# Kernel tuning notes

Hardware: AMD Instinct MI355X
Metric: run time of the kernel (lower is better)

Reference implementation:

```python
import jax, jax.numpy as jnp
import numpy as np
from jax import lax

B, L_IN, D, D_INNER = 4, 1024, 512, 512
H, DK = 8, 64
WIN = [4, 4, 4]
INNER_SIZE = 5   # temporal intra-level neighborhood size
SEM_K = 32       # opt.semantic_node: topk per level for semantic mask
N_LAYER = 2


def _build_temporal_mask(input_size, window_size, inner_size):
    # faithful port of Encoder.get_mask (Pyraformer-Naive mask)
    all_size = [input_size]
    for w in window_size:
        all_size.append(all_size[-1] // w)
    L = sum(all_size)
    m = np.zeros((L, L), dtype=np.float32)
    iw = inner_size // 2
    starts = [sum(all_size[:i]) for i in range(len(all_size))]
    for li, n in enumerate(all_size):
        st = starts[li]
        for i in range(st, st + n):
            m[i, max(i - iw, st):min(i + iw + 1, st + n)] = 1
    for li in range(1, len(all_size)):
        st = starts[li]
        prev = all_size[li - 1]
        w = window_size[li - 1]
        for i in range(st, st + all_size[li]):
            ls = st - prev + (i - st) * w
            rs = st if i == st + all_size[li] - 1 else st - prev + (i - st + 1) * w
            m[i, ls:rs] = 1
            m[ls:rs, i] = 1
    return (1 - m).astype(bool), all_size

TMASK_NP, ALL_SIZE = _build_temporal_mask(L_IN, WIN, INNER_SIZE)
L_TOT = sum(ALL_SIZE)  # 1360


def _ln(x, g, b, eps):
    mu = jnp.mean(x, axis=-1, keepdims=True)
    var = jnp.mean(jnp.square(x - mu), axis=-1, keepdims=True)
    return (x - mu) * lax.rsqrt(var + eps) * g + b


def _mha(x, Wq, Wk, Wv, fcW, fcb, g, b, mask):
    # post-norm MHA (normalize_before=False), dropout disabled (eval)
    Bq, L, _ = x.shape
    q = (x @ Wq).reshape(Bq, L, H, DK)
    k = (x @ Wk).reshape(Bq, L, H, DK)
    v = (x @ Wv).reshape(Bq, L, H, DK)
    a = jnp.einsum('bqhd,bkhd->bhqk', q, k) / np.float32(DK ** 0.5)
    a = jnp.where(mask, -jnp.inf, a)
    p = jax.nn.softmax(a, axis=-1)
    o = jnp.einsum('bhqk,bkhd->bqhd', p, v).reshape(Bq, L, H * DK)
    return _ln(o @ fcW + fcb + x, g, b, 1e-6)


def _semantic_mask(x):
    # get_semantic_mask: per-level cosine similarity, mask topk-most-similar within each level
    nrm = jnp.linalg.norm(x, axis=-1, keepdims=True)
    xn = x / jnp.maximum(nrm, 1e-8)
    sim = jnp.einsum('bid,bjd->bij', xn, xn)
    Bq = x.shape[0]
    mask = jnp.zeros((Bq, L_TOT, L_TOT), dtype=bool)
    bidx = jnp.arange(Bq)[:, None, None]
    start = 0
    for n in ALL_SIZE:
        k = min(n, SEM_K)
        blk = sim[:, start:start + n, start:start + n]
        idx = lax.top_k(blk, k)[1]              # [B, n, k]
        ridx = jnp.arange(n)[None, :, None]
        bm = jnp.zeros((Bq, n, n), dtype=bool).at[bidx, ridx, idx].set(True)
        mask = mask.at[:, start:start + n, start:start + n].set(bm)
        start += n
    return mask


def _bottleneck(x, dW, db, cW, cb, uW, ub, g, b):
    t = jnp.transpose(x @ dW + db, (0, 2, 1))  # [B, d_inner, L]
    outs = []
    for i in range(len(WIN)):
        t = lax.conv_general_dilated(t, cW[i], (WIN[i],), 'VALID',
                                     dimension_numbers=('NCH', 'OIH', 'NCH')) + cb[i][None, :, None]
        t = t / np.float32(np.sqrt(1.0 + 1e-5))  # eval BatchNorm with identity running stats
        t = jax.nn.elu(t)
        outs.append(t)
    pyr = jnp.transpose(jnp.concatenate(outs, axis=2), (0, 2, 1)) @ uW + ub
    return _ln(jnp.concatenate([x, pyr], axis=1), g, b, 1e-5)


def _forward(x_enc, down_W, down_b, conv_W, conv_b, up_W, up_b, bc_ln_g, bc_ln_b,
             attn_Wq, attn_Wk, attn_Wv, attn_fcW, attn_fcb, attn_ln_g, attn_ln_b,
             ffn_W1, ffn_b1, ffn_W2, ffn_b2, ffn_ln_g, ffn_ln_b):
    tmask = jnp.asarray(TMASK_NP)[None, None]  # [1,1,Lt,Lt]
    x = _bottleneck(x_enc, down_W, down_b, conv_W, conv_b, up_W, up_b, bc_ln_g, bc_ln_b)
    for l in range(N_LAYER):
        res = x
        t_out = _mha(x, attn_Wq[l, 0], attn_Wk[l, 0], attn_Wv[l, 0], attn_fcW[l, 0],
                     attn_fcb[l, 0], attn_ln_g[l, 0], attn_ln_b[l, 0], tmask)
        smask = _semantic_mask(x)[:, None]     # [B,1,Lt,Lt]
        s_out = _mha(x, attn_Wq[l, 1], attn_Wk[l, 1], attn_Wv[l, 1], attn_fcW[l, 1],
                     attn_fcb[l, 1], attn_ln_g[l, 1], attn_ln_b[l, 1], smask)
        x = (t_out + s_out + res) / 3.0
        res = x
        h = jax.nn.relu(x @ ffn_W1[l] + ffn_b1[l])
        x = _ln(h @ ffn_W2[l] + ffn_b2[l] + res, ffn_ln_g[l], ffn_ln_b[l], 1e-6)
    return x


def setup_inputs() -> dict:
    key = jax.random.key(0)
    ks = jax.random.split(key, 16)
    s = 0.02
    inp = {
        'x_enc': jax.random.normal(ks[0], (B, L_IN, D), jnp.float32),
        'down_W': jax.random.normal(ks[1], (D, D_INNER), jnp.float32) * s,
        'down_b': jnp.zeros((D_INNER,), jnp.float32),
        'conv_W': jax.random.normal(ks[2], (3, D_INNER, D_INNER, WIN[0]), jnp.float32) * s,
        'conv_b': jnp.zeros((3, D_INNER), jnp.float32),
        'up_W': jax.random.normal(ks[3], (D_INNER, D), jnp.float32) * s,
        'up_b': jnp.zeros((D,), jnp.float32),
        'bc_ln_g': jnp.ones((D,), jnp.float32),
        'bc_ln_b': jnp.zeros((D,), jnp.float32),
        'attn_Wq': jax.random.normal(ks[4], (N_LAYER, 2, D, H * DK), jnp.float32) * s,
        'attn_Wk': jax.random.normal(ks[5], (N_LAYER, 2, D, H * DK), jnp.float32) * s,
        'attn_Wv': jax.random.normal(ks[6], (N_LAYER, 2, D, H * DK), jnp.float32) * s,
        'attn_fcW': jax.random.normal(ks[7], (N_LAYER, 2, H * DK, D), jnp.float32) * s,
        'attn_fcb': jnp.zeros((N_LAYER, 2, D), jnp.float32),
        'attn_ln_g': jnp.ones((N_LAYER, 2, D), jnp.float32),
        'attn_ln_b': jnp.zeros((N_LAYER, 2, D), jnp.float32),
        'ffn_W1': jax.random.normal(ks[8], (N_LAYER, D, D_INNER), jnp.float32) * s,
        'ffn_b1': jnp.zeros((N_LAYER, D_INNER), jnp.float32),
        'ffn_W2': jax.random.normal(ks[9], (N_LAYER, D_INNER, D), jnp.float32) * s,
        'ffn_b2': jnp.zeros((N_LAYER, D), jnp.float32),
        'ffn_ln_g': jnp.ones((N_LAYER, D), jnp.float32),
        'ffn_ln_b': jnp.zeros((N_LAYER, D), jnp.float32),
    }
    return inp


def reference(x_enc, down_W, down_b, conv_W, conv_b, up_W, up_b, bc_ln_g, bc_ln_b,
              attn_Wq, attn_Wk, attn_Wv, attn_fcW, attn_fcb, attn_ln_g, attn_ln_b,
              ffn_W1, ffn_b1, ffn_W2, ffn_b2, ffn_ln_g, ffn_ln_b):
    return _forward(x_enc, down_W, down_b, conv_W, conv_b, up_W, up_b, bc_ln_g, bc_ln_b,
                    attn_Wq, attn_Wk, attn_Wv, attn_fcW, attn_fcb, attn_ln_g, attn_ln_b,
                    ffn_W1, ffn_b1, ffn_W2, ffn_b2, ffn_ln_g, ffn_ln_b)
```

## Files before the change

### kernel.cpp

```cpp
#include <hip/hip_runtime.h>
#include <float.h>
#include <math.h>
#include <stdint.h>

#define LT 1360
#define BB 4
#define DM 512
#define NHH 8
#define NBLE 2785280
#define MBW 24
#define QSCALE 0.18033688f
#define NFLASH 704

typedef __attribute__((ext_vector_type(8))) short short8;
typedef __attribute__((ext_vector_type(4))) float f32x4;
typedef unsigned long long u64;

__device__ __forceinline__ ushort f2b(float x){
    uint32_t u = __float_as_uint(x);
    return (ushort)((u + 0x7fffu + ((u >> 16) & 1u)) >> 16);
}
__device__ __forceinline__ float b2f(ushort u){
    return __uint_as_float(((uint32_t)u) << 16);
}
// ... 254 lines not shown
        bool nx = (k0 + 64 < K);
        if (nx){
            if (ABF){
                aR0 = *(const uint4*)(Ab + aoff + k0 + 64);
                aR1 = *(const uint4*)(Ab + aoff + k0 + 72);
            } else {
                f0  = *(const float4*)(Af + aoff + k0 + 64);
                f1  = *(const float4*)(Af + aoff + k0 + 68);
                f2v = *(const float4*)(Af + aoff + k0 + 72);
                f3v = *(const float4*)(Af + aoff + k0 + 76);
            }
            bR0 = *(const uint4*)(Bp + k0 + 64);
            bR1 = *(const uint4*)(Bp + k0 + 72);
        }
        __builtin_amdgcn_s_setprio(1);
        #pragma unroll
        for (int kk = 0; kk < 2; kk++){
            short8 af0 = *(const short8*)&As[wr + l15][(kk << 5) + (quad << 3)];
            short8 af1 = *(const short8*)&As[wr + 16 + l15][(kk << 5) + (quad << 3)];
            short8 bf0 = *(const short8*)&Bs[wc + l15][(kk << 5) + (quad << 3)];
            short8 bf1 = *(const short8*)&Bs[wc + 16 + l15][(kk << 5) + (quad << 3)];
            acc[0][0] = __builtin_amdgcn_mfma_f32_16x16x32_bf16(af0, bf0, acc[0][0], 0, 0, 0);
            acc[0][1] = __builtin_amdgcn_mfma_f32_16x16x32_bf16(af0, bf1, acc[0][1], 0, 0, 0);
            acc[1][0] = __builtin_amdgcn_mfma_f32_16x16x32_bf16(af1, bf0, acc[1][0], 0, 0, 0);
            acc[1][1] = __builtin_amdgcn_mfma_f32_16x16x32_bf16(af1, bf1, acc[1][1], 0, 0, 0);
        }
        __builtin_amdgcn_s_setprio(0);
        if (nx){
            __syncthreads();
            if (!ABF){
                aR0.x = (uint32_t)f2b(f0.x)  | ((uint32_t)f2b(f0.y)  << 16);
                aR0.y = (uint32_t)f2b(f0.z)  | ((uint32_t)f2b(f0.w)  << 16);
                aR0.z = (uint32_t)f2b(f1.x)  | ((uint32_t)f2b(f1.y)  << 16);
                aR0.w = (uint32_t)f2b(f1.z)  | ((uint32_t)f2b(f1.w)  << 16);
                aR1.x = (uint32_t)f2b(f2v.x) | ((uint32_t)f2b(f2v.y) << 16);
                aR1.y = (uint32_t)f2b(f2v.z) | ((uint32_t)f2b(f2v.w) << 16);
                aR1.z = (uint32_t)f2b(f3v.x) | ((uint32_t)f2b(f3v.y) << 16);
                aR1.w = (uint32_t)f2b(f3v.z) | ((uint32_t)f2b(f3v.w) << 16);
            }
            *(uint4*)&As[srow][sc]     = aR0;
            *(uint4*)&As[srow][sc + 8] = aR1;
            *(uint4*)&Bs[srow][sc]     = bR0;
            *(uint4*)&Bs[srow][sc + 8] = bR1;
            __syncthreads();
        }
    }
    #pragma unroll
    for (int mi = 0; mi < 2; mi++){
        #pragma unroll
        for (int r = 0; r < 4; r++){
            int row = gm + wr + (mi << 4) + (quad << 2) + r;
            #pragma unroll
            for (int ni = 0; ni < 2; ni++){
                int col = gn + wc + (ni << 4) + l15;
                float v = acc[mi][ni][r];
                if (bias) v += bias[col];
                if (Rres) v += Rres[(size_t)row * N + col];
                if (act == 2){ v = fmaxf(v, 0.f); }
                if (omode == 0){
                    int orow = mpb ? (row / mpb) * orpb + ooff + (row % mpb) : row;
                    ((float*)Cout)[(size_t)orow * N + col] = v;
                } else {
                    ((ushort*)Cout)[(size_t)row * N + col] = f2b(v);
                }
            }
        }
    }
}

__global__ __launch_bounds__(256)
void gemm_fc2(const ushort* __restrict__ A0, const ushort* __restrict__ A1,
              const ushort* __restrict__ B0, const ushort* __restrict__ B1,
              const float* __restrict__ bias0, const float* __restrict__ bias1,
              const float* __restrict__ Rres, float* __restrict__ C0,
              float* __restrict__ C1, int M, int N, int K)
{
    __shared__ ushort As[64][72];
    __shared__ ushort Bs[64][72];
    const ushort* Ab = blockIdx.z ? A1 : A0;
    const ushort* Bw = blockIdx.z ? B1 : B0;
    const float* bias = blockIdx.z ? bias1 : bias0;
    float* Cout = blockIdx.z ? C1 : C0;
    int tid = threadIdx.x;
    int lane = tid & 63, w = tid >> 6, quad = lane >> 4, l15 = lane & 15;
    int gm = blockIdx.y << 6, gn = blockIdx.x << 6;
    int wr = (w >> 1) << 5, wc = (w & 1) << 5;
    int srow = tid >> 2, sc = (tid & 3) << 4;
    f32x4 acc[2][2];
    #pragma unroll
    for (int mi = 0; mi < 2; mi++)
        #pragma unroll
        for (int ni = 0; ni < 2; ni++)
            acc[mi][ni] = (f32x4){0.f,0.f,0.f,0.f};
    size_t aoff = (size_t)(gm + srow) * K + sc;
    const ushort* Bp = Bw + (size_t)(gn + srow) * K + sc;
    uint4 aR0 = *(const uint4*)(Ab + aoff);
    uint4 aR1 = *(const uint4*)(Ab + aoff + 8);
    uint4 bR0 = *(const uint4*)(Bp);
    uint4 bR1 = *(const uint4*)(Bp + 8);
    *(uint4*)&As[srow][sc]     = aR0;
    *(uint4*)&As[srow][sc + 8] = aR1;
    *(uint4*)&Bs[srow][sc]     = bR0;
    *(uint4*)&Bs[srow][sc + 8] = bR1;
    __syncthreads();
    for (int k0 = 0; k0 < K; k0 += 64){
        bool nx = (k0 + 64 < K);
        if (nx){
            aR0 = *(const uint4*)(Ab + aoff + k0 + 64);
            aR1 = *(const uint4*)(Ab + aoff + k0 + 72);
            bR0 = *(const uint4*)(Bp + k0 + 64);
            bR1 = *(const uint4*)(Bp + k0 + 72);
        }
        __builtin_amdgcn_s_setprio(1);
        #pragma unroll
        for (int kk = 0; kk < 2; kk++){
            short8 af0 = *(const short8*)&As[wr + l15][(kk << 5) + (quad << 3)];
            short8 af1 = *(const short8*)&As[wr + 16 + l15][(kk << 5) + (quad << 3)];
            short8 bf0 = *(const short8*)&Bs[wc + l15][(kk << 5) + (quad << 3)];
            short8 bf1 = *(const short8*)&Bs[wc + 16 + l15][(kk << 5) + (quad << 3)];
            acc[0][0] = __builtin_amdgcn_mfma_f32_16x16x32_bf16(af0, bf0, acc[0][0], 0, 0, 0);
            acc[0][1] = __builtin_amdgcn_mfma_f32_16x16x32_bf16(af0, bf1, acc[0][1], 0, 0, 0);
            acc[1][0] = __builtin_amdgcn_mfma_f32_16x16x32_bf16(af1, bf0, acc[1][0], 0, 0, 0);
            acc[1][1] = __builtin_amdgcn_mfma_f32_16x16x32_bf16(af1, bf1, acc[1][1], 0, 0, 0);
        }
        __builtin_amdgcn_s_setprio(0);
        if (nx){
            __syncthreads();
            *(uint4*)&As[srow][sc]     = aR0;
            *(uint4*)&As[srow][sc + 8] = aR1;
            *(uint4*)&Bs[srow][sc]     = bR0;
            *(uint4*)&Bs[srow][sc + 8] = bR1;
            __syncthreads();
        }
    }
    #pragma unroll
    for (int mi = 0; mi < 2; mi++){
        #pragma unroll
        for (int r = 0; r < 4; r++){
            int row = gm + wr + (mi << 4) + (quad << 2) + r;
            #pragma unroll
            for (int ni = 0; ni < 2; ni++){
                int col = gn + wc + (ni << 4) + l15;
                float v = acc[mi][ni][r] + bias[col] + Rres[(size_t)row * N + col];
                Cout[(size_t)row * N + col] = v;
            }
        }
    }
}

__global__ __launch_bounds__(256)
void gemm_sk(const float* __restrict__ A, const ushort* __restrict__ Bw,
             float* __restrict__ P, int M, int N, int K, int kslice)
{
    __shared__ ushort As[64][40];
    __shared__ ushort Bs[64][40];
    int tid = threadIdx.x;
    int lane = tid & 63, w = tid >> 6, quad = lane >> 4, l15 = lane & 15;
    int gm = blockIdx.y << 6, gn = blockIdx.x << 6;
    int wr = (w >> 1) << 5, wc = (w & 1) << 5;
    int srow = tid >> 2, sc8 = (tid & 3) << 3;
    int ks = blockIdx.z * kslice;
    f32x4 acc[2][2];
    #pragma unroll
    for (int mi = 0; mi < 2; mi++)
        #pragma unroll
        for (int ni = 0; ni < 2; ni++)
            acc[mi][ni] = (f32x4){0.f,0.f,0.f,0.f};
    const float* Ap = A + (size_t)(gm + srow) * K;
    const ushort* Bp = Bw + (size_t)(gn + srow) * K;
    for (int k0 = ks; k0 < ks + kslice; k0 += 32){
        float4 a0 = *(const float4*)(Ap + k0 + sc8);
        float4 a1 = *(const float4*)(Ap + k0 + sc8 + 4);
        uint4 av;
        av.x = (uint32_t)f2b(a0.x) | ((uint32_t)f2b(a0.y) << 16);
        av.y = (uint32_t)f2b(a0.z) | ((uint32_t)f2b(a0.w) << 16);
        av.z = (uint32_t)f2b(a1.x) | ((uint32_t)f2b(a1.y) << 16);
        av.w = (uint32_t)f2b(a1.z) | ((uint32_t)f2b(a1.w) << 16);
        *(uint4*)&As[srow][sc8] = av;
        *(uint4*)&Bs[srow][sc8] = *(const uint4*)(Bp + k0 + sc8);
        __syncthreads();
        short8 af0 = *(const short8*)&As[wr + l15][quad << 3];
        short8 af1 = *(const short8*)&As[wr + 16 + l15][quad << 3];
        short8 bf0 = *(const short8*)&Bs[wc + l15][quad << 3];
        short8 bf1 = *(const short8*)&Bs[wc + 16 + l15][quad << 3];
        acc[0][0] = __builtin_amdgcn_mfma_f32_16x16x32_bf16(af0, bf0, acc[0][0], 0, 0, 0);
        acc[0][1] = __builtin_amdgcn_mfma_f32_16x16x32_bf16(af0, bf1, acc[0][1], 0, 0, 0);
        acc[1][0] = __builtin_amdgcn_mfma_f32_16x16x32_bf16(af1, bf0, acc[1][0], 0, 0, 0);
        acc[1][1] = __builtin_amdgcn_mfma_f32_16x16x32_bf16(af1, bf1, acc[1][1], 0, 0, 0);
        __syncthreads();
    }
    float* Pz = P + (size_t)blockIdx.z * M * N;
    #pragma unroll
    for (int mi = 0; mi < 2; mi++){
        #pragma unroll
        for (int r = 0; r < 4; r++){
            int row = gm + wr + (mi << 4) + (quad << 2) + r;
            #pragma unroll
            for (int ni = 0; ni < 2; ni++){
                int col = gn + wc + (ni << 4) + l15;
                Pz[(size_t)row * N + col] = acc[mi][ni][r];
            }
        }
    }
}

__global__ __launch_bounds__(256)
void sk_reduce(const float* __restrict__ P, const float* __restrict__ bias,
               float* __restrict__ C, int MN, int S)
{
    int idx = (blockIdx.x * 256 + threadIdx.x) << 2;
    if (idx >= MN) return;
    float4 s = {0.f, 0.f, 0.f, 0.f};
    for (int z = 0; z < S; z++){
        float4 v = *(const float4*)(P + (size_t)z * MN + idx);
        s.x += v.x; s.y += v.y; s.z += v.z; s.w += v.w;
    }
    const float cscale = 0.9999950000375f;
    int col = idx & 511;
    float o[4] = {s.x, s.y, s.z, s.w};
    #pragma unroll
    for (int t = 0; t < 4; t++){
        float v = (o[t] + bias[col + t]) * cscale;
        o[t] = (v > 0.f) ? v : expm1f(v);
    }
    *(float4*)(C + idx) = (float4){o[0], o[1], o[2], o[3]};
}

__global__ __launch_bounds__(256)
void sim_mfma(const ushort* __restrict__ XH, const ushort* __restrict__ XL,
              float* __restrict__ SIM){
    __shared__ ushort Ah[64][40], Al[64][40], Bh[64][40], Bl[64][40];
    int x = blockIdx.x, b = blockIdx.y;
    int ti, tj, st, n, goff;
    if (x < 256){ ti = x >> 4; tj = x & 15; st = 0; n = 1024; goff = SG0; }
    else if (x < 272){ int y = x - 256; ti = y >> 2; tj = y & 3; st = 1024; n = 256; goff = SG1; }
    else if (x == 272){ ti = 0; tj = 0; st = 1280; n = 64; goff = SG2; }
    else { ti = 0; tj = 0; st = 1344; n = 16; goff = SG3; }
    const ushort* XbH = XH + (((size_t)b * LT + st) << 9);
    const ushort* XbL = XL + (((size_t)b * LT + st) << 9);
    float* Cb = SIM + (size_t)b * SBT + goff;
    int gm = ti << 6, gn = tj << 6;
    int tid = threadIdx.x;
    int lane = tid & 63, w = tid >> 6, quad = lane >> 4, l15 = lane & 15;
    int wr = (w >> 1) << 5, wc = (w & 1) << 5;
    int srow = tid >> 2, sc8 = (tid & 3) << 3;
    int ra = gm + srow; if (ra > n - 1) ra = n - 1;
    int rb = gn + srow; if (rb > n - 1) rb = n - 1;
    f32x4 acc[2][2];
    #pragma unroll
    for (int mi = 0; mi < 2; mi++)
        #pragma unroll
        for (int ni = 0; ni < 2; ni++)
            acc[mi][ni] = (f32x4){0.f,0.f,0.f,0.f};
    const ushort* pAh = XbH + ((size_t)ra << 9) + sc8;
    const ushort* pAl = XbL + ((size_t)ra << 9) + sc8;
    const ushort* pBh = XbH + ((size_t)rb << 9) + sc8;
    const ushort* pBl = XbL + ((size_t)rb << 9) + sc8;
    uint4 vah = *(const uint4*)pAh;
    uint4 val = *(const uint4*)pAl;
    uint4 vbh = *(const uint4*)pBh;
    uint4 vbl = *(const uint4*)pBl;
    *(uint4*)&Ah[srow][sc8] = vah;
    *(uint4*)&Al[srow][sc8] = val;
    *(uint4*)&Bh[srow][sc8] = vbh;
    *(uint4*)&Bl[srow][sc8] = vbl;
    __syncthreads();
    for (int k0 = 0; k0 < 512; k0 += 32){
        bool nx = (k0 + 32 < 512);
        if (nx){
            vah = *(const uint4*)(pAh + k0 + 32);
            val = *(const uint4*)(pAl + k0 + 32);
            vbh = *(const uint4*)(pBh + k0 + 32);
            vbl = *(const uint4*)(pBl + k0 + 32);
        }
        __builtin_amdgcn_s_setprio(1);
        short8 ah0 = *(const short8*)&Ah[wr + l15][quad << 3];
        short8 ah1 = *(const short8*)&Ah[wr + 16 + l15][quad << 3];
        short8 al0 = *(const short8*)&Al[wr + l15][quad << 3];
        short8 al1 = *(const short8*)&Al[wr + 16 + l15][quad << 3];
        short8 bh0 = *(const short8*)&Bh[wc + l15][quad << 3];
        short8 bh1 = *(const short8*)&Bh[wc + 16 + l15][quad << 3];
        short8 bl0 = *(const short8*)&Bl[wc + l15][quad << 3];
        short8 bl1 = *(const short8*)&Bl[wc + 16 + l15][quad << 3];
        acc[0][0] = __builtin_amdgcn_mfma_f32_16x16x32_bf16(ah0, bh0, acc[0][0], 0, 0, 0);
        acc[0][0] = __builtin_amdgcn_mfma_f32_16x16x32_bf16(ah0, bl0, acc[0][0], 0, 0, 0);
        acc[0][0] = __builtin_amdgcn_mfma_f32_16x16x32_bf16(al0, bh0, acc[0][0], 0, 0, 0);
        acc[0][1] = __builtin_amdgcn_mfma_f32_16x16x32_bf16(ah0, bh1, acc[0][1], 0, 0, 0);
        acc[0][1] = __builtin_amdgcn_mfma_f32_16x16x32_bf16(ah0, bl1, acc[0][1], 0, 0, 0);
        acc[0][1] = __builtin_amdgcn_mfma_f32_16x16x32_bf16(al0, bh1, acc[0][1], 0, 0, 0);
        acc[1][0] = __builtin_amdgcn_mfma_f32_16x16x32_bf16(ah1, bh0, acc[1][0], 0, 0, 0);
        acc[1][0] = __builtin_amdgcn_mfma_f32_16x16x32_bf16(ah1, bl0, acc[1][0], 0, 0, 0);
        acc[1][0] = __builtin_amdgcn_mfma_f32_16x16x32_bf16(al1, bh0, acc[1][0], 0, 0, 0);
        acc[1][1] = __builtin_amdgcn_mfma_f32_16x16x32_bf16(ah1, bh1, acc[1][1], 0, 0, 0);
        acc[1][1] = __builtin_amdgcn_mfma_f32_16x16x32_bf16(ah1, bl1, acc[1][1], 0, 0, 0);
        acc[1][1] = __builtin_amdgcn_mfma_f32_16x16x32_bf16(al1, bh1, acc[1][1], 0, 0, 0);
        __builtin_amdgcn_s_setprio(0);
        if (nx){
            __syncthreads();
            *(uint4*)&Ah[srow][sc8] = vah;
            *(uint4*)&Al[srow][sc8] = val;
            *(uint4*)&Bh[srow][sc8] = vbh;
            *(uint4*)&Bl[srow][sc8] = vbl;
            __syncthreads();
        }
    }
    #pragma unroll
    for (int mi = 0; mi < 2; mi++){
        #pragma unroll
        for (int r = 0; r < 4; r++){
            int row = gm + wr + (mi << 4) + (quad << 2) + r;
            if (row < n){
                #pragma unroll
                for (int ni = 0; ni < 2; ni++){
                    int col = gn + wc + (ni << 4) + l15;
                    if (col < n) Cb[(size_t)row * n + col] = acc[mi][ni][r];
                }
            }
        }
    }
}

__global__ __launch_bounds__(256)
void pcat_copy(const float* __restrict__ C1, const float* __restrict__ C2,
               const float* __restrict__ C3, float* __restrict__ PC){
    int idx = blockIdx.x * 256 + threadIdx.x;
    int d = idx & 511;
    int r = (idx >> 9) % 336;
    int b = idx / (336 * 512);
    float v;
    if (r < 256)       v = C1[(((size_t)b * 256 + r) << 9) + d];
    else if (r < 320)  v = C2[(((size_t)b * 64 + (r - 256)) << 9) + d];
    else               v = C3[(((size_t)b * 16 + (r - 320)) << 9) + d];
    PC[idx] = v;
}

__global__ __launch_bounds__(256)
void xenc_copy(const float* __restrict__ xe, float* __restrict__ dst){
    int idx = blockIdx.x * 256 + threadIdx.x;
    int d = idx & 511;
    int l = (idx >> 9) & 1023;
    int b = idx >> 19;
    dst[(((size_t)b * LT + l) << 9) + d] = xe[idx];
// ... 41 lines not shown
        for (int t = 0; t < 8; t++){
            float v = nv[t] * inv;
            ushort h = f2b(v);
            qh[lane + t * 64] = h;
            ql[lane + t * 64] = f2b(v - b2f(h));
        }
    }
}

__global__ __launch_bounds__(256)
void ln2_add3(const float* __restrict__ in0, const float* __restrict__ in1,
              const float* __restrict__ g0, const float* __restrict__ b0,
              const float* __restrict__ g1, const float* __restrict__ b1,
              float* __restrict__ X, ushort* __restrict__ ob, float eps){
    int wid = threadIdx.x >> 6, lane = threadIdx.x & 63;
    int row = blockIdx.x * 4 + wid;
    const float* p0 = in0 + ((size_t)row << 9);
    const float* p1 = in1 + ((size_t)row << 9);
    float v0[8], v1[8];
    float s0 = 0.f, q0 = 0.f, s1 = 0.f, q1 = 0.f;
    #pragma unroll
    for (int t = 0; t < 8; t++){
        float a = p0[lane + t * 64]; v0[t] = a; s0 += a; q0 += a * a;
        float c = p1[lane + t * 64]; v1[t] = c; s1 += c; q1 += c * c;
    }
    #pragma unroll
    for (int off = 32; off; off >>= 1){
        s0 += __shfl_xor(s0, off, 64);
        q0 += __shfl_xor(q0, off, 64);
        s1 += __shfl_xor(s1, off, 64);
        q1 += __shfl_xor(q1, off, 64);
    }
    float mu0 = s0 * (1.f / 512.f);
    float r0 = rsqrtf(q0 * (1.f / 512.f) - mu0 * mu0 + eps);
    float mu1 = s1 * (1.f / 512.f);
    float r1 = rsqrtf(q1 * (1.f / 512.f) - mu1 * mu1 + eps);
    float* xp = X + ((size_t)row << 9);
    ushort* qb = ob + ((size_t)row << 9);
    #pragma unroll
    for (int t = 0; t < 8; t++){
        int c = lane + t * 64;
        float sn0 = (v0[t] - mu0) * r0 * g0[c] + b0[c];
        float sn1 = (v1[t] - mu1) * r1 * g1[c] + b1[c];
        float nv = (sn0 + sn1 + xp[c]) * (1.f / 3.f);
        xp[c] = nv;
        qb[c] = f2b(nv);
    }
}

__global__ __launch_bounds__(256)
void topk_sel(const float* __restrict__ SIM, u64* __restrict__ MB){
    int wid = threadIdx.x >> 6, lane = threadIdx.x & 63;
    int r = blockIdx.x * 4 + wid;
    int b = r / LT, i = r % LT;
    int bi, st, n; blk_info(i, bi, st, n);
    u64* mrow = MB + ((size_t)b * LT + i) * MBW;
    if (n == 16){
        u64 myw = 0;
        if (lane == 21) myw = ~0ULL;
        if (lane < MBW) mrow[lane] = myw;
        return;
    }
    int goff = (bi == 0) ? SG0 : (bi == 1) ? SG1 : SG2;
    const float* srow = SIM + (size_t)b * SBT + goff + (size_t)(i - st) * n;
    int ns = n >> 6;
    float vals[16];
    #pragma unroll
    for (int t = 0; t < 16; t++)
        vals[t] = (t < ns) ? srow[lane + (t << 6)] : -FLT_MAX;

    float c[32];
    #pragma unroll
    for (int t = 0; t < 16; t++) c[t] = vals[t];
    #pragma unroll
    for (int k = 2; k <= 16; k <<= 1){
        #pragma unroll
        for (int j = k >> 1; j > 0; j >>= 1){
            #pragma unroll
            for (int t = 0; t < 16; t++){
                int l = t ^ j;
                if (l > t){
                    float lo = fminf(c[t], c[l]);
                    float hi = fmaxf(c[t], c[l]);
                    if ((t & k) == 0){ c[t] = hi; c[l] = lo; }
                    else             { c[t] = lo; c[l] = hi; }
                }
            }
        }
    }
    #pragma unroll
    for (int t = 16; t < 32; t++) c[t] = -FLT_MAX;

    float V32;
    #pragma unroll
    for (int rd = 0; rd < 6; rd++){
        float f[32];
        #pragma unroll
        for (int t = 0; t < 32; t++) f[t] = __shfl_xor(c[t], 1 << rd, 64);
        float m[32];
        #pragma unroll
        for (int t = 0; t < 32; t++) m[t] = fmaxf(c[t], f[31 - t]);
        if (rd < 5){
            #pragma unroll
            for (int d = 16; d >= 1; d >>= 1){
                #pragma unroll
                for (int t = 0; t < 32; t++){
                    if ((t & d) == 0){
                        float lo = fminf(m[t], m[t + d]);
                        m[t] = fmaxf(m[t], m[t + d]);
                        m[t + d] = lo;
                    }
                }
            }
            #pragma unroll
            for (int t = 0; t < 32; t++) c[t] = m[t];
        } else {
            float mn = m[0];
            #pragma unroll
            for (int t = 1; t < 32; t++) mn = fminf(mn, m[t]);
            V32 = mn;
        }
    }

    int cnt_gt = 0;
    #pragma unroll
    for (int t = 0; t < 16; t++){
        u64 bg = __ballot(vals[t] > V32);
        cnt_gt += __popcll(bg);
    }
    int need = 32 - cnt_gt;
    u64 lmask = (1ULL << lane) - 1;
    u64 myw = 0;
    if (lane == 21) myw = 0xFFFFFFFFFFFF0000ULL;
    int eqrun = 0;
    int w0 = st >> 6;
    #pragma unroll
    for (int t = 0; t < 16; t++){
        bool eq = (vals[t] == V32);
        u64 beq = __ballot(eq);
        int below = __popcll(beq & lmask);
        bool sel = (vals[t] > V32) || (eq && (eqrun + below) < need);
        eqrun += __popcll(beq);
        u64 wsel = __ballot(sel);
        if (t < ns && lane == w0 + t) myw = wsel;
    }
    if (lane < MBW) mrow[lane] = myw;
}

__global__ __launch_bounds__(256)
void attn_fused(const ushort* __restrict__ U, const u64* __restrict__ MB,
                const int* __restrict__ IDX, const int* __restrict__ CNT,
                ushort* __restrict__ AO0, ushort* __restrict__ AO1)
{
    __shared__ ushort Ks[2][64][76];
    __shared__ ushort Vs[2][64][76];
    if (blockIdx.x < NFLASH){
        const ushort* Q  = U + (size_t)NBLE;
        const ushort* Kp = U + (size_t)3*NBLE;
        const ushort* Vt = U + (size_t)4*NBLE;
        int fid = blockIdx.x;
        int bh = fid & 31, b = bh >> 3, h = bh & 7;
        int q0 = (fid >> 5) << 6;
        int tid = threadIdx.x;
        int w = tid >> 6, lane = tid & 63, quad = lane >> 4, l15 = lane & 15;

        int qm = q0 + w * 16 + l15;
        int qmc = (qm < LT) ? qm : (LT - 1);
        const ushort* qp = Q + ((size_t)(b * LT + qmc) << 9) + h * 64 + (quad << 3);
        short8 qf0 = *(const short8*)qp;
        short8 qf1 = *(const short8*)(qp + 32);

        float l_part = 0.f;
        f32x4 Oacc[4];
        #pragma unroll
        for (int dt = 0; dt < 4; dt++) Oacc[dt] = (f32x4){0.f,0.f,0.f,0.f};

        int srow = tid >> 2, sc = (tid & 3) << 4;

        const ushort* kpp = Kp + ((size_t)(b * LT + srow) << 9) + h * 64 + sc;
        const ushort* vpp = Vt + (size_t)(b * 512 + h * 64 + srow) * LT + sc;
        const u64* mpp = MB + ((size_t)b * LT + qmc) * MBW;

        int srcA = ((quad & 1) << 5) + l15;
        int srcB = srcA + 16;
        bool ntHi = (quad & 2) != 0;

        {
            uint4 k0v = *(const uint4*)kpp;
            uint4 k1v = *(const uint4*)(kpp + 8);
            uint4 v0v = *(const uint4*)vpp;
            uint4 v1v = *(const uint4*)(vpp + 8);
            kpp += 64 * 512; vpp += 64;
            *(uint4*)&Ks[0][srow][sc]     = k0v;
            *(uint4*)&Ks[0][srow][sc + 8] = k1v;
            *(uint4*)&Vs[0][srow][sc]     = v0v;
            *(uint4*)&Vs[0][srow][sc + 8] = v1v;
        }
        __syncthreads();

        for (int kt = 0; kt < 22; kt++){
            int cur = kt & 1;
            bool havenext = (kt + 1 < 22);
            uint4 kn0, kn1, vn0, vn1;
            if (havenext){
                kn0 = *(const uint4*)kpp;
                kn1 = *(const uint4*)(kpp + 8);
                vn0 = *(const uint4*)vpp;
                vn1 = *(const uint4*)(vpp + 8);
                kpp += 64 * 512; vpp += 64;
            }
            u64 mw = mpp[kt];
            f32x4 s[4];
            #pragma unroll
            for (int nt = 0; nt < 4; nt++) s[nt] = (f32x4){0.f,0.f,0.f,0.f};
            __builtin_amdgcn_s_setprio(1);
            #pragma unroll
            for (int nt = 0; nt < 4; nt++){
                short8 kf0 = *(const short8*)&Ks[cur][(nt << 4) + l15][quad << 3];
                short8 kf1 = *(const short8*)&Ks[cur][(nt << 4) + l15][32 + (quad << 3)];
                s[nt] = __builtin_amdgcn_mfma_f32_16x16x32_bf16(kf0, qf0, s[nt], 0, 0, 0);
                s[nt] = __builtin_amdgcn_mfma_f32_16x16x32_bf16(kf1, qf1, s[nt], 0, 0, 0);
            }
            __builtin_amdgcn_s_setprio(0);
            u64 msh = mw >> (quad << 2);
            uint32_t pk01[4], pk23[4];
            #pragma unroll
            for (int nt = 0; nt < 4; nt++){
                float p0 = ((uint32_t)(msh >> (nt * 16 + 0)) & 1u) ? 0.f : ex2(s[nt][0]);
                float p1 = ((uint32_t)(msh >> (nt * 16 + 1)) & 1u) ? 0.f : ex2(s[nt][1]);
                float p2 = ((uint32_t)(msh >> (nt * 16 + 2)) & 1u) ? 0.f : ex2(s[nt][2]);
                float p3 = ((uint32_t)(msh >> (nt * 16 + 3)) & 1u) ? 0.f : ex2(s[nt][3]);
                l_part += (p0 + p1) + (p2 + p3);
                pk01[nt] = pkbf(p0, p1);
                pk23[nt] = pkbf(p2, p3);
            }
            uint4 pa, pb;
            {
                uint32_t t0, t1;
                t0 = __shfl(pk01[0], srcA, 64); t1 = __shfl(pk01[1], srcA, 64);
                pa.x = ntHi ? t1 : t0;
                t0 = __shfl(pk23[0], srcA, 64); t1 = __shfl(pk23[1], srcA, 64);
                pa.y = ntHi ? t1 : t0;
                t0 = __shfl(pk01[0], srcB, 64); t1 = __shfl(pk01[1], srcB, 64);
                pa.z = ntHi ? t1 : t0;
                t0 = __shfl(pk23[0], srcB, 64); t1 = __shfl(pk23[1], srcB, 64);
                pa.w = ntHi ? t1 : t0;
                t0 = __shfl(pk01[2], srcA, 64); t1 = __shfl(pk01[3], srcA, 64);
                pb.x = ntHi ? t1 : t0;
                t0 = __shfl(pk23[2], srcA, 64); t1 = __shfl(pk23[3], srcA, 64);
                pb.y = ntHi ? t1 : t0;
                t0 = __shfl(pk01[2], srcB, 64); t1 = __shfl(pk01[3], srcB, 64);
                pb.z = ntHi ? t1 : t0;
                t0 = __shfl(pk23[2], srcB, 64); t1 = __shfl(pk23[3], srcB, 64);
                pb.w = ntHi ? t1 : t0;
            }
            short8 pf0 = *(const short8*)&pa;
            short8 pf1 = *(const short8*)&pb;
            __builtin_amdgcn_s_setprio(1);
            #pragma unroll
            for (int dt = 0; dt < 4; dt++){
                short8 vf0 = *(const short8*)&Vs[cur][(dt << 4) + l15][quad << 3];
                short8 vf1 = *(const short8*)&Vs[cur][(dt << 4) + l15][32 + (quad << 3)];
                Oacc[dt] = __builtin_amdgcn_mfma_f32_16x16x32_bf16(pf0, vf0, Oacc[dt], 0, 0, 0);
                Oacc[dt] = __builtin_amdgcn_mfma_f32_16x16x32_bf16(pf1, vf1, Oacc[dt], 0, 0, 0);
            }
            __builtin_amdgcn_s_setprio(0);
            if (havenext){
                int nb = cur ^ 1;
                *(uint4*)&Ks[nb][srow][sc]     = kn0;
                *(uint4*)&Ks[nb][srow][sc + 8] = kn1;
                *(uint4*)&Vs[nb][srow][sc]     = vn0;
                *(uint4*)&Vs[nb][srow][sc + 8] = vn1;
            }
            __syncthreads();
        }
        l_part += __shfl_xor(l_part, 16, 64);
        l_part += __shfl_xor(l_part, 32, 64);
        #pragma unroll
        for (int r = 0; r < 4; r++){
            int qrow = q0 + (w << 4) + (quad << 2) + r;
            if (qrow < LT){
                float lr = __shfl(l_part, (lane & 48) + (quad << 2) + r, 64);
                float inv = 1.f / lr;
                #pragma unroll
                for (int dt = 0; dt < 4; dt++)
                    AO1[((size_t)(b * LT + qrow) << 9) + h * 64 + (dt << 4) + l15] =
                        f2b(Oacc[dt][r] * inv);
            }
        }
    } else {
        const ushort* Q  = U;
        const ushort* Kp = U + (size_t)2*NBLE;
        const ushort* Vn = U + (size_t)5*NBLE;
        int wid = threadIdx.x >> 6, lane = threadIdx.x & 63;
        int row = (blockIdx.x - NFLASH) * 4 + wid;
        int b = row / (NHH * LT);
        int rem = row % (NHH * LT);
        int h = rem / LT, i = rem % LT;
        int c = CNT[i];
        int quad = lane >> 4, l15 = lane & 15;
        int d0 = l15 << 2;
        int jl = IDX[i * 12 + (lane % 12)];
        const ushort* qp = Q + (((size_t)b * LT + i) << 9) + h * 64 + d0;
        uint2 qv = *(const uint2*)qp;
        float qd0 = b2f((ushort)qv.x), qd1 = b2f((ushort)(qv.x >> 16));
        float qd2 = b2f((ushort)qv.y), qd3 = b2f((ushort)(qv.y >> 16));
        const ushort* kb = Kp + (((size_t)b * LT) << 9) + h * 64 + d0;
        const ushort* vb = Vn + (((size_t)b * LT) << 9) + h * 64 + d0;
        float o0 = 0.f, o1 = 0.f, o2 = 0.f, o3 = 0.f;
        float lsum = 0.f;
        #pragma unroll
        for (int rr = 0; rr < 3; rr++){
            int t = (rr << 2) + quad;
            int j = __shfl(jl, t, 64);
            uint2 kv2 = *(const uint2*)(kb + ((size_t)j << 9));
            uint2 vv2 = *(const uint2*)(vb + ((size_t)j << 9));
            float s = qd0 * b2f((ushort)kv2.x) + qd1 * b2f((ushort)(kv2.x >> 16))
                    + qd2 * b2f((ushort)kv2.y) + qd3 * b2f((ushort)(kv2.y >> 16));
            s += __shfl_xor(s, 1, 64);
            s += __shfl_xor(s, 2, 64);
            s += __shfl_xor(s, 4, 64);
            s += __shfl_xor(s, 8, 64);
            float p = (t < c) ? ex2(s) : 0.f;
            lsum += p;
            o0 += p * b2f((ushort)vv2.x);
            o1 += p * b2f((ushort)(vv2.x >> 16));
            o2 += p * b2f((ushort)vv2.y);
            o3 += p * b2f((ushort)(vv2.y >> 16));
        }
        o0 += __shfl_xor(o0, 16, 64); o0 += __shfl_xor(o0, 32, 64);
        o1 += __shfl_xor(o1, 16, 64); o1 += __shfl_xor(o1, 32, 64);
        o2 += __shfl_xor(o2, 16, 64); o2 += __shfl_xor(o2, 32, 64);
        o3 += __shfl_xor(o3, 16, 64); o3 += __shfl_xor(o3, 32, 64);
        lsum += __shfl_xor(lsum, 16, 64);
        lsum += __shfl_xor(lsum, 32, 64);
        float inv = 1.f / lsum;
        if (quad == 0){
            uint2 ov;
            ov.x = pkbf(o0 * inv, o1 * inv);
            ov.y = pkbf(o2 * inv, o3 * inv);
            *(uint2*)(AO0 + (((size_t)b * LT + i) << 9) + h * 64 + d0) = ov;
        }
    }
}

extern "C" void kernel_launch(void* const* d_in, const int* in_sizes, int n_in,
                              void* d_out, int out_size, void* d_ws, size_t ws_size,
                              hipStream_t stream)
{
    const float* x_enc   = (const float*)d_in[0];
    const float* down_W  = (const float*)d_in[1];
    const float* down_b  = (const float*)d_in[2];
    const float* conv_W  = (const float*)d_in[3];
    const float* conv_b  = (const float*)d_in[4];
    const float* up_W    = (const float*)d_in[5];
    const float* up_b    = (const float*)d_in[6];
    const float* bc_g    = (const float*)d_in[7];
    const float* bc_b    = (const float*)d_in[8];
    const float* aWq     = (const float*)d_in[9];
    const float* aWk     = (const float*)d_in[10];
    const float* aWv     = (const float*)d_in[11];
    const float* afcW    = (const float*)d_in[12];
    const float* afcb    = (const float*)d_in[13];
    const float* alng    = (const float*)d_in[14];
    const float* alnb    = (const float*)d_in[15];
    const float* fW1     = (const float*)d_in[16];
    const float* fb1     = (const float*)d_in[17];
    const float* fW2     = (const float*)d_in[18];
    const float* fb2     = (const float*)d_in[19];
    const float* flng    = (const float*)d_in[20];
    const float* flnb    = (const float*)d_in[21];

    const size_t NBL = (size_t)NBLE;
    float* X   = (float*)d_ws;
    float* TMP = X   + NBL;
    float* Qb  = TMP + NBL;
    float* Kb  = Qb  + NBL;
    float* Vb  = Kb  + NBL;
    float* AO  = Vb  + NBL;
    float* TO  = AO  + NBL;
    float* SO  = TO  + NBL;
    u64* MBm = (u64*)(SO + NBL);
    int* TIDX = (int*)(MBm + (size_t)BB * LT * MBW);
    int* TCNT = TIDX + (size_t)LT * 12;
    ushort* WG = (ushort*)(TCNT + LT);
    const size_t M512 = 262144;
    ushort* WdownT = WG;                 size_t wo = M512;
    ushort* WupT   = WG + wo;            wo += M512;
    ushort* Wqkv   = WG + wo;            wo += 12 * M512;
    ushort* WfT    = WG + wo;            wo += 4 * M512;
    ushort* W1T    = WG + wo;            wo += 2 * M512;
    ushort* W2T    = WG + wo;            wo += 2 * M512;
    ushort* WCt    = WG + wo;            wo += 3 * 1048576;
    float* LP = (float*)(WG + wo);
    (void)LP;
    size_t need = 8 * NBL * sizeof(float) + (size_t)BB * LT * MBW * 8
                + (size_t)LT * 13 * 4 + wo * sizeof(ushort)
                + (size_t)2 * BB * NHH * LT * 4;
    if (ws_size < need) return;

    float* Y    = Qb;
    float* C1   = Kb;
    float* C2   = C1 + (size_t)BB*256*512;
    float* C3   = C2 + (size_t)BB*64*512;
    float* PCAT = Vb;
    float* SKP  = AO;
    ushort* XNh = (ushort*)AO;
    ushort* XNl = XNh + NBLE;
    float* SIMB = Qb;
    ushort* U   = (ushort*)Qb;
    ushort* XB  = (ushort*)SO;
    ushort* AOb0 = (ushort*)AO;
    ushort* AOb1 = AOb0 + NBLE;
    ushort* HfB = (ushort*)Qb;
    float* TMP1 = TO;

    auto gemmN = [&](const void* A, int abf, const ushort* Bw, const float* bias,
                     const float* res, void* C, int M,
                     int act, int omode, int mpb, int orpb, int ooff){
        dim3 grid(8, M / 64);
        if (abf) gemm64t<1><<<grid, 256, 0, stream>>>(A, Bw, bias, res, C, M, 512, 512,
                                                      act, omode, mpb, orpb, ooff);
        else     gemm64t<0><<<grid, 256, 0, stream>>>(A, Bw, bias, res, C, M, 512, 512,
                                                      act, omode, mpb, orpb, ooff);
    };
    auto convG = [&](const float* A, const ushort* Bw, const float* bias,
                     float* C, int M){
// ... 52 lines not shown
```

Before: 673.1 us.

## Prefetch split-K GEMM tiles with 64-wide K steps; single-buffer attention K/V

The split-K GEMM now stages a 64-wide K chunk per iteration instead of 32. The next chunk's global loads are issued before the MFMAs on the current chunk, and MFMA priority is raised around the compute. This halves the barrier count per K and overlaps loads with compute. Separately, the attention kernel switches from double-buffered to single-buffered K/V shared memory with two barriers per tile, which cuts LDS use (possibly raising occupancy) at the cost of an extra sync per iteration.

```diff
diff --git a/kernel.cpp b/kernel.cpp
--- a/kernel.cpp
+++ b/kernel.cpp
@@ -430,13 +430,13 @@
 void gemm_sk(const float* __restrict__ A, const ushort* __restrict__ Bw,
              float* __restrict__ P, int M, int N, int K, int kslice)
 {
-    __shared__ ushort As[64][40];
-    __shared__ ushort Bs[64][40];
+    __shared__ ushort As[64][72];
+    __shared__ ushort Bs[64][72];
     int tid = threadIdx.x;
     int lane = tid & 63, w = tid >> 6, quad = lane >> 4, l15 = lane & 15;
     int gm = blockIdx.y << 6, gn = blockIdx.x << 6;
     int wr = (w >> 1) << 5, wc = (w & 1) << 5;
-    int srow = tid >> 2, sc8 = (tid & 3) << 3;
+    int srow = tid >> 2, sc = (tid & 3) << 4;
     int ks = blockIdx.z * kslice;
     f32x4 acc[2][2];
     #pragma unroll
@@ -444,28 +444,68 @@
         #pragma unroll
         for (int ni = 0; ni < 2; ni++)
             acc[mi][ni] = (f32x4){0.f,0.f,0.f,0.f};
-    const float* Ap = A + (size_t)(gm + srow) * K;
-    const ushort* Bp = Bw + (size_t)(gn + srow) * K;
-    for (int k0 = ks; k0 < ks + kslice; k0 += 32){
-        float4 a0 = *(const float4*)(Ap + k0 + sc8);
-        float4 a1 = *(const float4*)(Ap + k0 + sc8 + 4);
-        uint4 av;
-        av.x = (uint32_t)f2b(a0.x) | ((uint32_t)f2b(a0.y) << 16);
-        av.y = (uint32_t)f2b(a0.z) | ((uint32_t)f2b(a0.w) << 16);
-        av.z = (uint32_t)f2b(a1.x) | ((uint32_t)f2b(a1.y) << 16);
-        av.w = (uint32_t)f2b(a1.z) | ((uint32_t)f2b(a1.w) << 16);
-        *(uint4*)&As[srow][sc8] = av;
-        *(uint4*)&Bs[srow][sc8] = *(const uint4*)(Bp + k0 + sc8);
-        __syncthreads();
-        short8 af0 = *(const short8*)&As[wr + l15][quad << 3];
-        short8 af1 = *(const short8*)&As[wr + 16 + l15][quad << 3];
-        short8 bf0 = *(const short8*)&Bs[wc + l15][quad << 3];
-        short8 bf1 = *(const short8*)&Bs[wc + 16 + l15][quad << 3];
-        acc[0][0] = __builtin_amdgcn_mfma_f32_16x16x32_bf16(af0, bf0, acc[0][0], 0, 0, 0);
-        acc[0][1] = __builtin_amdgcn_mfma_f32_16x16x32_bf16(af0, bf1, acc[0][1], 0, 0, 0);
-        acc[1][0] = __builtin_amdgcn_mfma_f32_16x16x32_bf16(af1, bf0, acc[1][0], 0, 0, 0);
-        acc[1][1] = __builtin_amdgcn_mfma_f32_16x16x32_bf16(af1, bf1, acc[1][1], 0, 0, 0);
-        __syncthreads();
+    size_t aoff = (size_t)(gm + srow) * K + ks + sc;
+    const ushort* Bp = Bw + (size_t)(gn + srow) * K + ks + sc;
+    uint4 aR0, aR1, bR0, bR1;
+    float4 f0, f1, f2v, f3v;
+    f0  = *(const float4*)(A + aoff);
+    f1  = *(const float4*)(A + aoff + 4);
+    f2v = *(const float4*)(A + aoff + 8);
+    f3v = *(const float4*)(A + aoff + 12);
+    bR0 = *(const uint4*)(Bp);
+    bR1 = *(const uint4*)(Bp + 8);
+    aR0.x = (uint32_t)f2b(f0.x)  | ((uint32_t)f2b(f0.y)  << 16);
+    aR0.y = (uint32_t)f2b(f0.z)  | ((uint32_t)f2b(f0.w)  << 16);
+    aR0.z = (uint32_t)f2b(f1.x)  | ((uint32_t)f2b(f1.y)  << 16);
+    aR0.w = (uint32_t)f2b(f1.z)  | ((uint32_t)f2b(f1.w)  << 16);
+    aR1.x = (uint32_t)f2b(f2v.x) | ((uint32_t)f2b(f2v.y) << 16);
+    aR1.y = (uint32_t)f2b(f2v.z) | ((uint32_t)f2b(f2v.w) << 16);
+    aR1.z = (uint32_t)f2b(f3v.x) | ((uint32_t)f2b(f3v.y) << 16);
+    aR1.w = (uint32_t)f2b(f3v.z) | ((uint32_t)f2b(f3v.w) << 16);
+    *(uint4*)&As[srow][sc]     = aR0;
+    *(uint4*)&As[srow][sc + 8] = aR1;
+    *(uint4*)&Bs[srow][sc]     = bR0;
+    *(uint4*)&Bs[srow][sc + 8] = bR1;
+    __syncthreads();
+    for (int kc = 0; kc < kslice; kc += 64){
+        bool nx = (kc + 64 < kslice);
+        if (nx){
+            f0  = *(const float4*)(A + aoff + kc + 64);
+            f1  = *(const float4*)(A + aoff + kc + 68);
+            f2v = *(const float4*)(A + aoff + kc + 72);
+            f3v = *(const float4*)(A + aoff + kc + 76);
+            bR0 = *(const uint4*)(Bp + kc + 64);
+            bR1 = *(const uint4*)(Bp + kc + 72);
+        }
+        __builtin_amdgcn_s_setprio(1);
+        #pragma unroll
+        for (int kk = 0; kk < 2; kk++){
+            short8 af0 = *(const short8*)&As[wr + l15][(kk << 5) + (quad << 3)];
+            short8 af1 = *(const short8*)&As[wr + 16 + l15][(kk << 5) + (quad << 3)];
+            short8 bf0 = *(const short8*)&Bs[wc + l15][(kk << 5) + (quad << 3)];
+            short8 bf1 = *(const short8*)&Bs[wc + 16 + l15][(kk << 5) + (quad << 3)];
+            acc[0][0] = __builtin_amdgcn_mfma_f32_16x16x32_bf16(af0, bf0, acc[0][0], 0, 0, 0);
+            acc[0][1] = __builtin_amdgcn_mfma_f32_16x16x32_bf16(af0, bf1, acc[0][1], 0, 0, 0);
+            acc[1][0] = __builtin_amdgcn_mfma_f32_16x16x32_bf16(af1, bf0, acc[1][0], 0, 0, 0);
+            acc[1][1] = __builtin_amdgcn_mfma_f32_16x16x32_bf16(af1, bf1, acc[1][1], 0, 0, 0);
+        }
+        __builtin_amdgcn_s_setprio(0);
+        if (nx){
+            __syncthreads();
+            aR0.x = (uint32_t)f2b(f0.x)  | ((uint32_t)f2b(f0.y)  << 16);
+            aR0.y = (uint32_t)f2b(f0.z)  | ((uint32_t)f2b(f0.w)  << 16);
+            aR0.z = (uint32_t)f2b(f1.x)  | ((uint32_t)f2b(f1.y)  << 16);
+            aR0.w = (uint32_t)f2b(f1.z)  | ((uint32_t)f2b(f1.w)  << 16);
+            aR1.x = (uint32_t)f2b(f2v.x) | ((uint32_t)f2b(f2v.y) << 16);
+            aR1.y = (uint32_t)f2b(f2v.z) | ((uint32_t)f2b(f2v.w) << 16);
+            aR1.z = (uint32_t)f2b(f3v.x) | ((uint32_t)f2b(f3v.y) << 16);
+            aR1.w = (uint32_t)f2b(f3v.z) | ((uint32_t)f2b(f3v.w) << 16);
+            *(uint4*)&As[srow][sc]     = aR0;
+            *(uint4*)&As[srow][sc + 8] = aR1;
+            *(uint4*)&Bs[srow][sc]     = bR0;
+            *(uint4*)&Bs[srow][sc + 8] = bR1;
+            __syncthreads();
+        }
     }
     float* Pz = P + (size_t)blockIdx.z * M * N;
     #pragma unroll
@@ -813,8 +853,8 @@
                 const int* __restrict__ IDX, const int* __restrict__ CNT,
                 ushort* __restrict__ AO0, ushort* __restrict__ AO1)
 {
-    __shared__ ushort Ks[2][64][76];
-    __shared__ ushort Vs[2][64][76];
+    __shared__ ushort Ks[64][76];
+    __shared__ ushort Vs[64][76];
     if (blockIdx.x < NFLASH){
         const ushort* Q  = U + (size_t)NBLE;
         const ushort* Kp = U + (size_t)3*NBLE;
@@ -852,15 +892,14 @@
             uint4 v0v = *(const uint4*)vpp;
             uint4 v1v = *(const uint4*)(vpp + 8);
             kpp += 64 * 512; vpp += 64;
-            *(uint4*)&Ks[0][srow][sc]     = k0v;
-            *(uint4*)&Ks[0][srow][sc + 8] = k1v;
-            *(uint4*)&Vs[0][srow][sc]     = v0v;
-            *(uint4*)&Vs[0][srow][sc + 8] = v1v;
+            *(uint4*)&Ks[srow][sc]     = k0v;
+            *(uint4*)&Ks[srow][sc + 8] = k1v;
+            *(uint4*)&Vs[srow][sc]     = v0v;
+            *(uint4*)&Vs[srow][sc + 8] = v1v;
         }
         __syncthreads();
 
         for (int kt = 0; kt < 22; kt++){
-            int cur = kt & 1;
             bool havenext = (kt + 1 < 22);
             uint4 kn0, kn1, vn0, vn1;
             if (havenext){
@@ -877,8 +916,8 @@
             __builtin_amdgcn_s_setprio(1);
             #pragma unroll
             for (int nt = 0; nt < 4; nt++){
-                short8 kf0 = *(const short8*)&Ks[cur][(nt << 4) + l15][quad << 3];
-                short8 kf1 = *(const short8*)&Ks[cur][(nt << 4) + l15][32 + (quad << 3)];
+                short8 kf0 = *(const short8*)&Ks[(nt << 4) + l15][quad << 3];
+                short8 kf1 = *(const short8*)&Ks[(nt << 4) + l15][32 + (quad << 3)];
                 s[nt] = __builtin_amdgcn_mfma_f32_16x16x32_bf16(kf0, qf0, s[nt], 0, 0, 0);
                 s[nt] = __builtin_amdgcn_mfma_f32_16x16x32_bf16(kf1, qf1, s[nt], 0, 0, 0);
             }
@@ -920,20 +959,20 @@
             __builtin_amdgcn_s_setprio(1);
             #pragma unroll
             for (int dt = 0; dt < 4; dt++){
-                short8 vf0 = *(const short8*)&Vs[cur][(dt << 4) + l15][quad << 3];
-                short8 vf1 = *(const short8*)&Vs[cur][(dt << 4) + l15][32 + (quad << 3)];
+                short8 vf0 = *(const short8*)&Vs[(dt << 4) + l15][quad << 3];
+                short8 vf1 = *(const short8*)&Vs[(dt << 4) + l15][32 + (quad << 3)];
                 Oacc[dt] = __builtin_amdgcn_mfma_f32_16x16x32_bf16(pf0, vf0, Oacc[dt], 0, 0, 0);
                 Oacc[dt] = __builtin_amdgcn_mfma_f32_16x16x32_bf16(pf1, vf1, Oacc[dt], 0, 0, 0);
             }
             __builtin_amdgcn_s_setprio(0);
             if (havenext){
-                int nb = cur ^ 1;
-                *(uint4*)&Ks[nb][srow][sc]     = kn0;
-                *(uint4*)&Ks[nb][srow][sc + 8] = kn1;
-                *(uint4*)&Vs[nb][srow][sc]     = vn0;
-                *(uint4*)&Vs[nb][srow][sc + 8] = vn1;
-            }
-            __syncthreads();
+                __syncthreads();
+                *(uint4*)&Ks[srow][sc]     = kn0;
+                *(uint4*)&Ks[srow][sc + 8] = kn1;
+                *(uint4*)&Vs[srow][sc]     = vn0;
+                *(uint4*)&Vs[srow][sc + 8] = vn1;
+                __syncthreads();
+            }
         }
         l_part += __shfl_xor(l_part, 16, 64);
         l_part += __shfl_xor(l_part, 32, 64);
```

Result: slower. 693.4 us (+3.0%).
